# Performance work log

Hardware: AMD Instinct MI355X
Metric: run time of the kernel (lower is better)

## Reference

```python
import jax, jax.numpy as jnp
import numpy as np
import math

B, T, C, H, L, V = 4, 2048, 256, 4, 2, 1024
HS = C // H  # head size


def setup_inputs() -> dict:
    key = jax.random.key(0)
    ks = jax.random.split(key, 10)
    s = 0.02
    return {
        "tokens": jax.random.randint(ks[0], (B, T), 0, V),
        "wte": s * jax.random.normal(ks[1], (V + 1, C), dtype=jnp.float32),
        "ln1_g": jnp.ones((L, C), jnp.float32),
        "ln1_b": jnp.zeros((L, C), jnp.float32),
        "attn_w": s * jax.random.normal(ks[2], (L, 3 * C, C), dtype=jnp.float32),
        "attn_b": jnp.zeros((L, 3 * C), jnp.float32),
        "proj_w": s * jax.random.normal(ks[3], (L, C, C), dtype=jnp.float32),
        "proj_b": jnp.zeros((L, C), jnp.float32),
        "embk": s * jax.random.normal(ks[4], (L, T, HS), dtype=jnp.float32),
        "embv": s * jax.random.normal(ks[5], (L, T, HS), dtype=jnp.float32),
        "ln2_g": jnp.ones((L, C), jnp.float32),
        "ln2_b": jnp.zeros((L, C), jnp.float32),
        "fc_w": s * jax.random.normal(ks[6], (L, 4 * C, C), dtype=jnp.float32),
        "fc_b": jnp.zeros((L, 4 * C), jnp.float32),
        "mproj_w": s * jax.random.normal(ks[7], (L, C, 4 * C), dtype=jnp.float32),
        "mproj_b": jnp.zeros((L, C), jnp.float32),
        "lnf_g": jnp.ones((C,), jnp.float32),
        "lnf_b": jnp.zeros((C,), jnp.float32),
        "head_w": s * jax.random.normal(ks[8], (V, C), dtype=jnp.float32),
    }


def _ln(x, g, b):
    mu = x.mean(-1, keepdims=True)
    var = x.var(-1, keepdims=True)
    return (x - mu) / jnp.sqrt(var + 1e-5) * g + b


def _gelu(x):  # NewGELU (tanh approximation)
    return 0.5 * x * (1.0 + jnp.tanh(math.sqrt(2.0 / math.pi) * (x + 0.044715 * x ** 3)))


def reference(tokens, wte, ln1_g, ln1_b, attn_w, attn_b, proj_w, proj_b,
              embk, embv, ln2_g, ln2_b, fc_w, fc_b, mproj_w, mproj_b,
              lnf_g, lnf_b, head_w):
    x = wte[tokens]  # [B,T,C]; no absolute pos emb in this model
    idx = jnp.arange(T)
    rel = jnp.tril(idx[:, None] - idx[None, :])  # [T,T] nonneg offsets
    causal = idx[:, None] >= idx[None, :]
    scale = 1.0 / math.sqrt(HS)
    for l in range(L):
        h = _ln(x, ln1_g[l], ln1_b[l])
        qkv = h @ attn_w[l].T + attn_b[l]  # [B,T,3C]
        q, k, v = jnp.split(qkv, 3, axis=-1)
        q = q.reshape(B, T, H, HS).transpose(0, 2, 1, 3)  # [B,H,T,hs]
        k = k.reshape(B, T, H, HS).transpose(0, 2, 1, 3)
        v = v.reshape(B, T, H, HS).transpose(0, 2, 1, 3)
        rk = embk[l][rel]  # [T,T,hs]
        rv = embv[l][rel]  # [T,T,hs]
        att = jnp.einsum('bhtd,bhsd->bhts', q, k) * scale \
            + jnp.einsum('bhtd,tsd->bhts', q, rk)
        att = jnp.where(causal, att, -jnp.inf)
        att = jax.nn.softmax(att, axis=-1)
        y = jnp.einsum('bhts,bhsd->bhtd', att, v) \
            + jnp.einsum('bhts,tsd->bhtd', att, rv)
        y = y.transpose(0, 2, 1, 3).reshape(B, T, C)
        x = x + (y @ proj_w[l].T + proj_b[l])
        h2 = _ln(x, ln2_g[l], ln2_b[l])
        x = x + (_gelu(h2 @ fc_w[l].T + fc_b[l]) @ mproj_w[l].T + mproj_b[l])
    x = _ln(x, lnf_g, lnf_b)
    return x @ head_w.T  # [B,T,V] logits
```

## Files before the change

kernel.cpp:

```cpp
#include <hip/hip_runtime.h>
#include <hip/hip_bf16.h>
#include <math.h>

#define BB 4
#define TT 2048
#define CC 256
#define HH 4
#define LL 2
#define VV 1024
#define HS 64
#define EPAD 2176
#define LOG2E 1.4426950408889634f

typedef __attribute__((ext_vector_type(8))) __bf16 bf16x8;
typedef __attribute__((ext_vector_type(4))) float f32x4;

#define MFMA16(a, b, c) __builtin_amdgcn_mfma_f32_16x16x32_bf16((a), (b), (c), 0, 0, 0)

__device__ __forceinline__ ushort f2bf(float f) {
    __hip_bfloat16 h = __float2bfloat16(f);
    return *reinterpret_cast<ushort*>(&h);
}
__device__ __forceinline__ float bf2f(ushort u) {
    union { uint i; float f; } c; c.i = ((uint)u) << 16; return c.f;
}

__device__ __forceinline__ void gload16(const void* g, void* l) {
    __builtin_amdgcn_global_load_lds(
        (const __attribute__((address_space(1))) void*)g,
        (__attribute__((address_space(3))) void*)l, 16, 0, 0);
}

__device__ __forceinline__ float gelu_f(float v) {
    return 0.5f * v * (1.0f + tanhf(0.7978845608028654f * (v + 0.044715f * v * v * v)));
}

__global__ void prep_kernel(const float* __restrict__ w0, const float* __restrict__ w1,
                            const float* __restrict__ w2, const float* __restrict__ w3,
                            const float* __restrict__ w4,
                            ushort* __restrict__ o0, ushort* __restrict__ o1,
                            ushort* __restrict__ o2, ushort* __restrict__ o3,
                            ushort* __restrict__ o4,
                            const float* __restrict__ ek, const float* __restrict__ ev,
                            ushort* __restrict__ ekp, ushort* __restrict__ evtp) {
    int bi = blockIdx.x;
    if (bi < 1792) {
        int i = bi * 256 + threadIdx.x;
        const float* src; ushort* dst; int j;
        if (i < 98304)       { src = w0; dst = o0; j = i; }
        else if (i < 131072) { src = w1; dst = o1; j = i - 98304; }
        else if (i < 262144) { src = w2; dst = o2; j = i - 131072; }
        else if (i < 393216) { src = w3; dst = o3; j = i - 262144; }
        else                 { src = w4; dst = o4; j = i - 393216; }
        float4 v = ((const float4*)src)[j];
        ushort4 o;
        o.x = f2bf(v.x); o.y = f2bf(v.y); o.z = f2bf(v.z); o.w = f2bf(v.w);
        ((ushort4*)dst)[j] = o;
    } else {
        int i = (bi - 1792) * 256 + threadIdx.x;
        int l = i / (EPAD * 64);
        int j = i - l * (EPAD * 64);
        int rp = j >> 6, d = j & 63;
        int o = rp - 64;
        bool in = (o >= 0 && o < TT);
        float kv = in ? ek[(size_t)l * TT * HS + (size_t)o * 64 + d] * LOG2E : 0.0f;
        float vv = in ? ev[(size_t)l * TT * HS + (size_t)o * 64 + d] : 0.0f;
        ekp[(size_t)l * EPAD * 64 + (size_t)rp * 64 + d] = f2bf(kv);
        evtp[(size_t)l * 64 * EPAD + (size_t)d * EPAD + rp] = f2bf(vv);
    }
}

__global__ __launch_bounds__(256) void embed_ln_kernel(
        const int* __restrict__ tok, const float* __restrict__ wte,
        const float* __restrict__ g, const float* __restrict__ b,
        float* __restrict__ x, ushort* __restrict__ h) {
    int row = blockIdx.x * 4 + (threadIdx.x >> 6);
    int lane = threadIdx.x & 63;
    int tk = tok[row];
    float4 v = ((const float4*)(wte + (size_t)tk * CC))[lane];
    float s = v.x + v.y + v.z + v.w;
    float s2 = v.x * v.x + v.y * v.y + v.z * v.z + v.w * v.w;
    for (int m = 1; m < 64; m <<= 1) {
        s += __shfl_xor(s, m);
        s2 += __shfl_xor(s2, m);
    }
    float mean = s * (1.0f / CC);
    float var = s2 * (1.0f / CC) - mean * mean;
    float rs = rsqrtf(var + 1e-5f);
    float4 gg = ((const float4*)g)[lane];
    float4 bb = ((const float4*)b)[lane];
    ushort4 o;
    o.x = f2bf((v.x - mean) * rs * gg.x + bb.x);
    o.y = f2bf((v.y - mean) * rs * gg.y + bb.y);
    o.z = f2bf((v.z - mean) * rs * gg.z + bb.z);
    o.w = f2bf((v.w - mean) * rs * gg.w + bb.w);
    ((float4*)(x + (size_t)row * CC))[lane] = v;
    ((ushort4*)(h + (size_t)row * CC))[lane] = o;
}

template<int MODE>
__global__ __launch_bounds__(512) void bgemm256_kernel(
        const ushort* __restrict__ A, const ushort* __restrict__ W,
        const float* __restrict__ bias, float* __restrict__ out,
        ushort* __restrict__ outb, int N, int K,
        ushort* __restrict__ qb, ushort* __restrict__ kb,
        ushort* __restrict__ vtb) {
    constexpr int BUFSH = 16 * 512;
    __shared__ ushort lds[3 * BUFSH];
    int tid = threadIdx.x;
    int w = tid >> 6, lane = tid & 63;
    int lo = lane & 15, hi = lane >> 4;
    int row0 = blockIdx.y * 128;
    int col0 = blockIdx.x * 128;
    int wm = w >> 2, wn = w & 3;
    const ushort* Asrc = A + (size_t)row0 * K;
    const ushort* Wsrc = W + (size_t)col0 * K;

    auto STAGE = [&](int buf, int k0) {
        ushort* dst = &lds[buf * BUFSH];
        gload16(Asrc + (size_t)(w * 16 + lo) * K + k0 + hi * 8, dst + w * 512);
        gload16(Wsrc + (size_t)(w * 16 + lo) * K + k0 + hi * 8, dst + (8 + w) * 512);
    };

    f32x4 acc[4][2] = {};
    int NT = K >> 5;
    STAGE(0, 0);
    STAGE(1, 32);
    int cur = 0;
    for (int t = 0; t < NT; ++t) {
        if (t + 1 < NT) asm volatile("s_waitcnt vmcnt(2)" ::: "memory");
        else            asm volatile("s_waitcnt vmcnt(0)" ::: "memory");
        __syncthreads();
        if (t + 2 < NT) {
            int st = cur ? cur - 1 : 2;
            STAGE(st, (t + 2) << 5);
        }
        bf16x8 a[4], b[2];
#pragma unroll
        for (int f = 0; f < 4; ++f)
            a[f] = *(const bf16x8*)&lds[cur * BUFSH + (wm * 4 + f) * 512 + lane * 8];
#pragma unroll
        for (int g = 0; g < 2; ++g)
            b[g] = *(const bf16x8*)&lds[cur * BUFSH + (8 + wn * 2 + g) * 512 + lane * 8];
        __builtin_amdgcn_s_setprio(1);
#pragma unroll
        for (int f = 0; f < 4; ++f)
#pragma unroll
            for (int g = 0; g < 2; ++g)
                acc[f][g] = MFMA16(a[f], b[g], acc[f][g]);
        __builtin_amdgcn_s_setprio(0);
        cur = cur < 2 ? cur + 1 : 0;
    }
#pragma unroll
    for (int f = 0; f < 4; ++f) {
        int rr = row0 + wm * 64 + f * 16 + hi * 4;
#pragma unroll
        for (int g = 0; g < 2; ++g) {
            int cc = col0 + wn * 32 + g * 16 + lo;
            float bv = bias ? bias[cc] : 0.0f;
#pragma unroll
            for (int j = 0; j < 4; ++j) {
                int r = rr + j;
                float v = acc[f][g][j] + bv;
                if (MODE == 3) {
                    int t = r & 2047, bb2 = r >> 11;
                    int which = cc >> 8, hh = (cc >> 6) & 3, dd = cc & 63;
                    size_t bh = (size_t)(bb2 * 4 + hh);
                    if (which == 0)      qb[(bh * 2048 + t) * 64 + dd] = f2bf(v);
                    else if (which == 1) kb[(bh * 2048 + t) * 64 + dd] = f2bf(v * (0.125f * LOG2E));
                    else                 vtb[(bh * 64 + dd) * 2048 + t] = f2bf(v);
                } else if (MODE == 2) {
                    outb[(size_t)r * N + cc] = f2bf(gelu_f(v));
                } else {
                    out[(size_t)r * N + cc] = v;
                }
            }
        }
    }
}

template<int NSTEP>
__global__ __launch_bounds__(512) void bgemmln_kernel(
        const ushort* __restrict__ A, const ushort* __restrict__ W,
        const float* __restrict__ bias, float* __restrict__ x,
        const float* __restrict__ lng, const float* __restrict__ lnb,
        ushort* __restrict__ hout) {
    extern __shared__ ushort plds[];
    constexpr int K = NSTEP * 64;
    constexpr int BUFSH = 36 * 512;
    int tid = threadIdx.x;
    int w = tid >> 6, lane = tid & 63;
    int lo = lane & 15, hi = lane >> 4;
    int row0 = blockIdx.x * 32;
    int wm = w >> 2, wn = w & 3;
    const ushort* Asrc = A + (size_t)row0 * K;

    auto STAGE = [&](int buf, int k0) {
        ushort* dst = &plds[buf * BUFSH];
        for (int s = w; s < 36; s += 8) {
            const ushort* src;
            if (s < 4) {
                int rg = s >> 1, kh = s & 1;
                src = Asrc + (size_t)(rg * 16 + lo) * K + k0 + kh * 32 + hi * 8;
            } else {
                int sb = s - 4, cg = sb >> 1, kh = sb & 1;
                src = W + (size_t)(cg * 16 + lo) * K + k0 + kh * 32 + hi * 8;
            }
            gload16(src, dst + s * 512);
        }
    };

    f32x4 acc[4] = {};
    STAGE(0, 0);
    STAGE(1, 64);
    int cur = 0;
    for (int t = 0; t < NSTEP; ++t) {
        if (t + 1 < NSTEP) {
            if (w < 4) asm volatile("s_waitcnt vmcnt(5)" ::: "memory");
            else       asm volatile("s_waitcnt vmcnt(4)" ::: "memory");
        } else {
            asm volatile("s_waitcnt vmcnt(0)" ::: "memory");
        }
        __syncthreads();
        if (t + 2 < NSTEP) {
            int st = cur ? cur - 1 : 2;
            STAGE(st, (t + 2) << 6);
        }
        bf16x8 a[2];
#pragma unroll
        for (int kh = 0; kh < 2; ++kh)
            a[kh] = *(const bf16x8*)&plds[cur * BUFSH + (wm * 2 + kh) * 512 + lane * 8];
        __builtin_amdgcn_s_setprio(1);
#pragma unroll
        for (int g2 = 0; g2 < 4; ++g2) {
#pragma unroll
            for (int kh = 0; kh < 2; ++kh) {
                bf16x8 b = *(const bf16x8*)&plds[cur * BUFSH + 2048 +
                                                 ((wn * 4 + g2) * 2 + kh) * 512 + lane * 8];
                acc[g2] = MFMA16(a[kh], b, acc[g2]);
            }
        }
        __builtin_amdgcn_s_setprio(0);
        cur = cur < 2 ? cur + 1 : 0;
    }

    float* part = (float*)&plds[3 * BUFSH];
    float v[4][4];
    float s1[4] = {0, 0, 0, 0}, s2[4] = {0, 0, 0, 0};
#pragma unroll
    for (int g2 = 0; g2 < 4; ++g2) {
        int cc = wn * 64 + g2 * 16 + lo;
        float bv = bias[cc];
#pragma unroll
        for (int j = 0; j < 4; ++j) {
            int r = row0 + wm * 16 + hi * 4 + j;
            float tv = acc[g2][j] + bv + x[(size_t)r * CC + cc];
            v[g2][j] = tv;
            s1[j] += tv;
            s2[j] += tv * tv;
        }
    }
#pragma unroll
    for (int msk = 1; msk < 16; msk <<= 1)
#pragma unroll
        for (int j = 0; j < 4; ++j) {
            s1[j] += __shfl_xor(s1[j], msk);
            s2[j] += __shfl_xor(s2[j], msk);
        }
    if (lo == 0) {
#pragma unroll
        for (int j = 0; j < 4; ++j) {
            int rr = wm * 16 + hi * 4 + j;
            part[rr * 4 + wn] = s1[j];
            part[128 + rr * 4 + wn] = s2[j];
        }
    }
    __syncthreads();
#pragma unroll
    for (int j = 0; j < 4; ++j) {
        int rr = wm * 16 + hi * 4 + j;
        int r = row0 + rr;
        float4 p1 = *(float4*)&part[rr * 4];
        float4 p2 = *(float4*)&part[128 + rr * 4];
        float mean = (p1.x + p1.y + p1.z + p1.w) * (1.0f / CC);
        float var = (p2.x + p2.y + p2.z + p2.w) * (1.0f / CC) - mean * mean;
        float rsd = rsqrtf(var + 1e-5f);
#pragma unroll
        for (int g2 = 0; g2 < 4; ++g2) {
            int cc = wn * 64 + g2 * 16 + lo;
            x[(size_t)r * CC + cc] = v[g2][j];
            hout[(size_t)r * CC + cc] =
                f2bf((v[g2][j] - mean) * rsd * lng[cc] + lnb[cc]);
        }
    }
}

#define SBUF 57344
#define KOFF 0
#define VOFF 8192
#define EKOFF 16384
#define EVOFF 32768
#define WSCR (2 * SBUF)

__global__ __launch_bounds__(512, 2) void flash_kernel(
        const ushort* __restrict__ qb,
        const ushort* __restrict__ kb,
        const ushort* __restrict__ vtb,
        const ushort* __restrict__ ekp,
        const ushort* __restrict__ evtp,
        ushort* __restrict__ y) {
    extern __shared__ __align__(16) char dls[];

    int g = blockIdx.x;
    int lbid = ((g & 7) << 5) | (g >> 3);
    int bh = lbid >> 4;
    int pk = lbid & 15;
    int tid = threadIdx.x;
    int w = tid >> 6;
    int sub = w & 3;
    int h = w >> 2;
    int lane = tid & 63;
    int lo = lane & 15, hi = lane >> 4;
    int sw = (lo & 7) << 4;

    char* wbase = dls + WSCR + w * 6144;
    ushort (*Rl)[88]   = (ushort (*)[88])  wbase;
    ushort (*Pl)[72]   = (ushort (*)[72])  wbase;
    ushort (*Ppl)[104] = (ushort (*)[104])(wbase + 2816);

    {
        uint* pz = reinterpret_cast<uint*>(&Ppl[0][0]);
        for (int i = lane; i < 832; i += 64) pz[i] = 0;
    }

    const char* kB  = (const char*)(kb  + (size_t)bh * 2048 * 64);
    const char* vB  = (const char*)(vtb + (size_t)bh * 64 * 2048);
    const char* ekB = (const char*)ekp;
    const char* evB = (const char*)evtp;

    int t0A = (31 - pk) * 64, t0B = pk * 64;
    int NSA = 32 - pk;
    const int NC = 33;

    auto STAGE = [&](int buf, int ci) {
        int t0 = (ci < NSA) ? t0A : t0B;
        int s0 = ((ci < NSA) ? ci : ci - NSA) * 64;
        int band0 = t0 - s0;
        char* B = dls + buf * SBUF;
        int wb = (tid & 448) << 4;
        {
            int gb = tid * 16;
            int r = gb >> 7, c = gb & 127;
            gload16(kB + (size_t)(s0 + r) * 128 + (c ^ ((r & 7) << 4)), B + KOFF + wb);
        }
        {
            int gb = tid * 16;
            int r = gb >> 7, c = gb & 127;
            gload16(vB + (size_t)r * 4096 + (size_t)s0 * 2 + (c ^ ((r & 7) << 4)),
                    B + VOFF + wb);
        }
#pragma unroll
        for (int p = 0; p < 2; ++p) {
            int gb = p * 8192 + tid * 16;
            int r = gb >> 7, c = gb & 127;
            gload16(ekB + (size_t)(band0 + r) * 128 + (c ^ ((r & 7) << 4)),
                    B + EKOFF + p * 8192 + wb);
        }
#pragma unroll
        for (int p = 0; p < 3; ++p) {
            int gb = p * 8192 + tid * 16;
            int r = gb / 384, c = gb - r * 384;
            gload16(evB + (size_t)r * 4352 + (size_t)band0 * 2 + (c ^ ((r & 7) << 4)),
                    B + EVOFF + p * 8192 + wb);
        }
    };

    STAGE(0, 0);
    asm volatile("s_waitcnt vmcnt(0)" ::: "memory");
    __syncthreads();

    int b_ = bh >> 2, h_ = bh & 3;
    int buf = 0, ci = 0;
    int nb = h ? 0 : 2;
    int kcA = h ? 0 : 1, kcB = h ? 1 : 2;

    for (int tile = 0; tile < 2; ++tile) {
        int t0 = tile ? t0B : t0A;
        int NS = tile ? (pk + 1) : NSA;

        const ushort* qbase = qb + ((size_t)bh * 2048 + t0 + sub * 16) * 64;
        bf16x8 qf0 = *(const bf16x8*)(qbase + (size_t)lo * 64 + hi * 8);
        bf16x8 qf1 = *(const bf16x8*)(qbase + (size_t)lo * 64 + 32 + hi * 8);

        float rs[4] = {0.0f, 0.0f, 0.0f, 0.0f};
        f32x4 O[4] = {};

        for (int c = 0; c < NS; ++c, ++ci) {
            if (ci + 1 < NC) STAGE(buf ^ 1, ci + 1);
            const char* B = dls + buf * SBUF;
            bool diag = (c == NS - 1);

            f32x4 sacc[2] = {};
            __builtin_amdgcn_s_setprio(1);
#pragma unroll
            for (int ni = 0; ni < 2; ++ni) {
                int R = (2 * h + ni) * 16 + lo;
                bf16x8 b0 = *(const bf16x8*)(B + KOFF + R * 128 + ((hi * 16) ^ sw));
                bf16x8 b1 = *(const bf16x8*)(B + KOFF + R * 128 + ((64 + hi * 16) ^ sw));
                sacc[ni] = MFMA16(qf0, b0, sacc[ni]);
                sacc[ni] = MFMA16(qf1, b1, sacc[ni]);
            }
#pragma unroll
            for (int ni = 0; ni < 3; ++ni) {
                int n = nb + ni;
                int RL = (sub + n) * 16 + lo;
                f32x4 r = {};
                bf16x8 e0 = *(const bf16x8*)(B + EKOFF + RL * 128 + ((hi * 16) ^ sw));
                bf16x8 e1 = *(const bf16x8*)(B + EKOFF + RL * 128 + ((64 + hi * 16) ^ sw));
                r = MFMA16(qf0, e0, r);
                r = MFMA16(qf1, e1, r);
#pragma unroll
                for (int j = 0; j < 4; ++j) Rl[hi * 4 + j][n * 16 + lo] = f2bf(r[j]);
            }
            __builtin_amdgcn_s_setprio(0);
            float sv[2][4];
#pragma unroll
            for (int ni = 0; ni < 2; ++ni) {
                int sl = (2 * h + ni) * 16 + lo;
#pragma unroll
                for (int j = 0; j < 4; ++j) {
                    int r_ = hi * 4 + j;
                    sv[ni][j] = sacc[ni][j] + bf2f(Rl[r_][r_ - sl + 64]);
                }
            }
            asm volatile("" ::: "memory");
#pragma unroll
            for (int ni = 0; ni < 2; ++ni) {
                int sl = (2 * h + ni) * 16 + lo;
#pragma unroll
                for (int j = 0; j < 4; ++j) {
                    int r_ = hi * 4 + j;
                    float p = (!diag || sl <= sub * 16 + r_) ? exp2f(sv[ni][j]) : 0.0f;
                    rs[j] += p;
                    ushort pu = f2bf(p);
                    Pl[r_][sl] = pu;
                    Ppl[r_][r_ - sl + 64] = pu;
                }
            }
            asm volatile("" ::: "memory");

            __builtin_amdgcn_s_setprio(1);
            bf16x8 pa  = *(const bf16x8*)(&Pl[lo][h * 32 + hi * 8]);
            bf16x8 pb0 = *(const bf16x8*)(&Ppl[lo][kcA * 32 + hi * 8]);
            bf16x8 pb1 = *(const bf16x8*)(&Ppl[lo][kcB * 32 + hi * 8]);
#pragma unroll
            for (int n = 0; n < 4; ++n) {
                int R = n * 16 + lo;
                bf16x8 bv = *(const bf16x8*)(B + VOFF + R * 128 + ((h * 64 + hi * 16) ^ sw));
                O[n] = MFMA16(pa, bv, O[n]);
                bf16x8 e0 = *(const bf16x8*)(B + EVOFF + R * 384 +
                                             ((sub * 32 + kcA * 64 + hi * 16) ^ sw));
                O[n] = MFMA16(pb0, e0, O[n]);
                bf16x8 e1 = *(const bf16x8*)(B + EVOFF + R * 384 +
                                             ((sub * 32 + kcB * 64 + hi * 16) ^ sw));
                O[n] = MFMA16(pb1, e1, O[n]);
            }
            __builtin_amdgcn_s_setprio(0);
            asm volatile("" ::: "memory");

            asm volatile("s_waitcnt vmcnt(0)" ::: "memory");
            __syncthreads();
            buf ^= 1;
        }

#pragma unroll
        for (int msk = 1; msk < 16; msk <<= 1)
#pragma unroll
            for (int j = 0; j < 4; ++j) rs[j] += __shfl_xor(rs[j], msk);

        char* mscr = dls + (buf ^ 1) * SBUF + sub * 8192;
        if (h == 1) {
            float* Of = (float*)mscr;
#pragma unroll
            for (int n = 0; n < 4; ++n)
#pragma unroll
                for (int j = 0; j < 4; ++j)
                    Of[(hi * 4 + j) * 64 + n * 16 + lo] = O[n][j];
            if (lo == 0)
#pragma unroll
                for (int j = 0; j < 4; ++j)
                    ((float*)(mscr + 4096))[hi * 4 + j] = rs[j];
        }
        __syncthreads();
        if (h == 0) {
            float* Of = (float*)mscr;
            float inv[4];
#pragma unroll
            for (int j = 0; j < 4; ++j)
                inv[j] = 1.0f / (rs[j] + ((float*)(mscr + 4096))[hi * 4 + j]);
#pragma unroll
            for (int n = 0; n < 4; ++n)
#pragma unroll
                for (int j = 0; j < 4; ++j) {
                    int r = t0 + sub * 16 + hi * 4 + j;
                    float v = O[n][j] + Of[(hi * 4 + j) * 64 + n * 16 + lo];
                    y[((size_t)(b_ * 2048 + r)) * 256 + h_ * 64 + n * 16 + lo] =
                        f2bf(v * inv[j]);
                }
        }
        __syncthreads();
    }
}

extern "C" void kernel_launch(void* const* d_in, const int* in_sizes, int n_in,
                              void* d_out, int out_size, void* d_ws, size_t ws_size,
                              hipStream_t stream) {
    const int*   tokens  = (const int*)d_in[0];
    const float* wte     = (const float*)d_in[1];
    const float* ln1_g   = (const float*)d_in[2];
    const float* ln1_b   = (const float*)d_in[3];
    const float* attn_w  = (const float*)d_in[4];
    const float* attn_b  = (const float*)d_in[5];
    const float* proj_w  = (const float*)d_in[6];
    const float* proj_b  = (const float*)d_in[7];
    const float* embk    = (const float*)d_in[8];
    const float* embv    = (const float*)d_in[9];
    const float* ln2_g   = (const float*)d_in[10];
    const float* ln2_b   = (const float*)d_in[11];
    const float* fc_w    = (const float*)d_in[12];
    const float* fc_b    = (const float*)d_in[13];
    const float* mproj_w = (const float*)d_in[14];
    const float* mproj_b = (const float*)d_in[15];
    const float* lnf_g   = (const float*)d_in[16];
    const float* lnf_b   = (const float*)d_in[17];
    const float* head_w  = (const float*)d_in[18];
    float* out = (float*)d_out;

    const int M = BB * TT;
    char* wsb = (char*)d_ws;
    float*  x    = (float*)wsb;
    ushort* h    = (ushort*)(wsb + ((size_t)8 << 20));
    ushort* y    = (ushort*)(wsb + ((size_t)12 << 20));
    ushort* qb   = (ushort*)(wsb + ((size_t)16 << 20));
    ushort* kbf  = (ushort*)(wsb + ((size_t)20 << 20));
    ushort* vtb  = (ushort*)(wsb + ((size_t)24 << 20));
    ushort* ekp  = (ushort*)(wsb + ((size_t)28 << 20));
    ushort* evtp = ekp + (size_t)LL * EPAD * 64;
    ushort* attn_wb  = (ushort*)(wsb + ((size_t)30 << 20));
    ushort* proj_wb  = attn_wb + (size_t)LL * 3 * CC * CC;
    ushort* fc_wb    = proj_wb + (size_t)LL * CC * CC;
    ushort* mproj_wb = fc_wb + (size_t)LL * 4 * CC * CC;
    ushort* head_wb  = mproj_wb + (size_t)LL * CC * 4 * CC;
    ushort* fcb = (ushort*)d_out;

    dim3 blk(256);
    const int FLDS = WSCR + 8 * 6144;
    const int PLDS = 3 * 36864 + 1024;
    hipFuncSetAttribute(reinterpret_cast<const void*>(flash_kernel),
                        hipFuncAttributeMaxDynamicSharedMemorySize, FLDS);
    hipFuncSetAttribute(reinterpret_cast<const void*>(bgemmln_kernel<4>),
                        hipFuncAttributeMaxDynamicSharedMemorySize, PLDS);
    hipFuncSetAttribute(reinterpret_cast<const void*>(bgemmln_kernel<16>),
                        hipFuncAttributeMaxDynamicSharedMemorySize, PLDS);

    prep_kernel<<<dim3(2880), blk, 0, stream>>>(
        attn_w, proj_w, fc_w, mproj_w, head_w,
        attn_wb, proj_wb, fc_wb, mproj_wb, head_wb,
        embk, embv, ekp, evtp);

    embed_ln_kernel<<<dim3(M / 4), blk, 0, stream>>>(
        tokens, wte, ln1_g, ln1_b, x, h);

    for (int l = 0; l < LL; l++) {
        bgemm256_kernel<3><<<dim3(6, 64), dim3(512), 0, stream>>>(
            h, attn_wb + (size_t)l * 3 * CC * CC, attn_b + (size_t)l * 3 * CC,
            nullptr, nullptr, 3 * CC, CC, qb, kbf, vtb);
        flash_kernel<<<dim3(256), dim3(512), FLDS, stream>>>(
            qb, kbf, vtb, ekp + (size_t)l * EPAD * 64, evtp + (size_t)l * 64 * EPAD, y);
        bgemmln_kernel<4><<<dim3(256), dim3(512), PLDS, stream>>>(
            y, proj_wb + (size_t)l * CC * CC, proj_b + (size_t)l * CC,
            x, ln2_g + l * CC, ln2_b + l * CC, h);
        bgemm256_kernel<2><<<dim3(8, 64), dim3(512), 0, stream>>>(
            h, fc_wb + (size_t)l * 4 * CC * CC, fc_b + (size_t)l * 4 * CC,
            nullptr, fcb, 4 * CC, CC, nullptr, nullptr, nullptr);
        const float* ng = (l == 0) ? (ln1_g + CC) : lnf_g;
        const float* nb = (l == 0) ? (ln1_b + CC) : lnf_b;
        bgemmln_kernel<16><<<dim3(256), dim3(512), PLDS, stream>>>(
            fcb, mproj_wb + (size_t)l * CC * 4 * CC, mproj_b + (size_t)l * CC,
            x, ng, nb, h);
    }

    bgemm256_kernel<0><<<dim3(8, 64), dim3(512), 0, stream>>>(
        h, head_wb, nullptr, out, nullptr, VV, CC, nullptr, nullptr, nullptr);
}
```

Measured before the change: 325.3 us.

## Split KV staging into two phases with finer-grained vmcnt waits

Result: no change. 323.9 us, median of 2 (-0.4%).

```diff
diff --git a/kernel.cpp b/kernel.cpp
--- a/kernel.cpp
+++ b/kernel.cpp
@@ -342,7 +342,7 @@
     int NSA = 32 - pk;
     const int NC = 33;
 
-    auto STAGE = [&](int buf, int ci) {
+    auto STAGE_KE = [&](int buf, int ci) {
         int t0 = (ci < NSA) ? t0A : t0B;
         int s0 = ((ci < NSA) ? ci : ci - NSA) * 64;
         int band0 = t0 - s0;
@@ -353,6 +353,20 @@
             int r = gb >> 7, c = gb & 127;
             gload16(kB + (size_t)(s0 + r) * 128 + (c ^ ((r & 7) << 4)), B + KOFF + wb);
         }
+#pragma unroll
+        for (int p = 0; p < 2; ++p) {
+            int gb = p * 8192 + tid * 16;
+            int r = gb >> 7, c = gb & 127;
+            gload16(ekB + (size_t)(band0 + r) * 128 + (c ^ ((r & 7) << 4)),
+                    B + EKOFF + p * 8192 + wb);
+        }
+    };
+    auto STAGE_VE = [&](int buf, int ci) {
+        int t0 = (ci < NSA) ? t0A : t0B;
+        int s0 = ((ci < NSA) ? ci : ci - NSA) * 64;
+        int band0 = t0 - s0;
+        char* B = dls + buf * SBUF;
+        int wb = (tid & 448) << 4;
         {
             int gb = tid * 16;
             int r = gb >> 7, c = gb & 127;
@@ -360,13 +374,6 @@
                     B + VOFF + wb);
         }
 #pragma unroll
-        for (int p = 0; p < 2; ++p) {
-            int gb = p * 8192 + tid * 16;
-            int r = gb >> 7, c = gb & 127;
-            gload16(ekB + (size_t)(band0 + r) * 128 + (c ^ ((r & 7) << 4)),
-                    B + EKOFF + p * 8192 + wb);
-        }
-#pragma unroll
         for (int p = 0; p < 3; ++p) {
             int gb = p * 8192 + tid * 16;
             int r = gb / 384, c = gb - r * 384;
@@ -375,30 +382,37 @@
         }
     };
 
-    STAGE(0, 0);
-    asm volatile("s_waitcnt vmcnt(0)" ::: "memory");
-    __syncthreads();
+    const ushort* qbaseA = qb + ((size_t)bh * 2048 + t0A + sub * 16) * 64;
+    const ushort* qbaseB = qb + ((size_t)bh * 2048 + t0B + sub * 16) * 64;
+    bf16x8 qfA0 = *(const bf16x8*)(qbaseA + (size_t)lo * 64 + hi * 8);
+    bf16x8 qfA1 = *(const bf16x8*)(qbaseA + (size_t)lo * 64 + 32 + hi * 8);
+    bf16x8 qfB0 = *(const bf16x8*)(qbaseB + (size_t)lo * 64 + hi * 8);
+    bf16x8 qfB1 = *(const bf16x8*)(qbaseB + (size_t)lo * 64 + 32 + hi * 8);
+    STAGE_KE(0, 0);
+    STAGE_VE(0, 0);
 
     int b_ = bh >> 2, h_ = bh & 3;
-    int buf = 0, ci = 0;
+    int ci = 0;
     int nb = h ? 0 : 2;
     int kcA = h ? 0 : 1, kcB = h ? 1 : 2;
 
     for (int tile = 0; tile < 2; ++tile) {
         int t0 = tile ? t0B : t0A;
         int NS = tile ? (pk + 1) : NSA;
-
-        const ushort* qbase = qb + ((size_t)bh * 2048 + t0 + sub * 16) * 64;
-        bf16x8 qf0 = *(const bf16x8*)(qbase + (size_t)lo * 64 + hi * 8);
-        bf16x8 qf1 = *(const bf16x8*)(qbase + (size_t)lo * 64 + 32 + hi * 8);
+        bf16x8 qf0 = tile ? qfB0 : qfA0;
+        bf16x8 qf1 = tile ? qfB1 : qfA1;
 
         float rs[4] = {0.0f, 0.0f, 0.0f, 0.0f};
         f32x4 O[4] = {};
 
         for (int c = 0; c < NS; ++c, ++ci) {
-            if (ci + 1 < NC) STAGE(buf ^ 1, ci + 1);
-            const char* B = dls + buf * SBUF;
+            int cur = ci & 1;
+            const char* B = dls + cur * SBUF;
             bool diag = (c == NS - 1);
+
+            asm volatile("s_waitcnt vmcnt(4)" ::: "memory");
+            __syncthreads();
+            if (ci + 1 < NC) STAGE_KE(cur ^ 1, ci + 1);
 
             f32x4 sacc[2] = {};
             __builtin_amdgcn_s_setprio(1);
@@ -448,6 +462,11 @@
                 }
             }
             asm volatile("" ::: "memory");
+
+            if (ci + 1 < NC) asm volatile("s_waitcnt vmcnt(3)" ::: "memory");
+            else             asm volatile("s_waitcnt vmcnt(0)" ::: "memory");
+            __syncthreads();
+            if (ci + 1 < NC) STAGE_VE(cur ^ 1, ci + 1);
 
             __builtin_amdgcn_s_setprio(1);
             bf16x8 pa  = *(const bf16x8*)(&Pl[lo][h * 32 + hi * 8]);
@@ -467,10 +486,6 @@
             }
             __builtin_amdgcn_s_setprio(0);
             asm volatile("" ::: "memory");
-
-            asm volatile("s_waitcnt vmcnt(0)" ::: "memory");
-            __syncthreads();
-            buf ^= 1;
         }
 
 #pragma unroll
@@ -478,7 +493,8 @@
 #pragma unroll
             for (int j = 0; j < 4; ++j) rs[j] += __shfl_xor(rs[j], msk);
 
-        char* mscr = dls + (buf ^ 1) * SBUF + sub * 8192;
+        char* mscr = dls + ((ci - 1) & 1) * SBUF + sub * 8192;
+        __syncthreads();
         if (h == 1) {
             float* Of = (float*)mscr;
 #pragma unroll
```

## Split flash attention into one query tile per block and read rel-pos embeddings from global

Applied to the files above, without the earlier changes.

Result: slower. 439.0 us (+35.0%).

```diff
diff --git a/kernel.cpp b/kernel.cpp
--- a/kernel.cpp
+++ b/kernel.cpp
@@ -295,14 +295,12 @@
     }
 }
 
-#define SBUF 57344
-#define KOFF 0
-#define VOFF 8192
-#define EKOFF 16384
-#define EVOFF 32768
-#define WSCR (2 * SBUF)
-
-__global__ __launch_bounds__(512, 2) void flash_kernel(
+#define FKOFF 0
+#define FVOFF 8192
+#define FSTG 16384
+#define FWSCR 32768
+
+__global__ __launch_bounds__(512, 4) void flash_kernel(
         const ushort* __restrict__ qb,
         const ushort* __restrict__ kb,
         const ushort* __restrict__ vtb,
@@ -312,9 +310,13 @@
     extern __shared__ __align__(16) char dls[];
 
     int g = blockIdx.x;
-    int lbid = ((g & 7) << 5) | (g >> 3);
-    int bh = lbid >> 4;
-    int pk = lbid & 15;
+    int phase = g >> 8;
+    int pk = (g >> 4) & 15;
+    int bh = g & 15;
+    int tile = phase ? pk : (31 - pk);
+    int t0 = tile * 64;
+    int NS = tile + 1;
+
     int tid = threadIdx.x;
     int w = tid >> 6;
     int sub = w & 3;
@@ -323,7 +325,7 @@
     int lo = lane & 15, hi = lane >> 4;
     int sw = (lo & 7) << 4;
 
-    char* wbase = dls + WSCR + w * 6144;
+    char* wbase = dls + FWSCR + w * 6144;
     ushort (*Rl)[88]   = (ushort (*)[88])  wbase;
     ushort (*Pl)[72]   = (ushort (*)[72])  wbase;
     ushort (*Ppl)[104] = (ushort (*)[104])(wbase + 2816);
@@ -333,182 +335,146 @@
         for (int i = lane; i < 832; i += 64) pz[i] = 0;
     }
 
-    const char* kB  = (const char*)(kb  + (size_t)bh * 2048 * 64);
-    const char* vB  = (const char*)(vtb + (size_t)bh * 64 * 2048);
-    const char* ekB = (const char*)ekp;
-    const char* evB = (const char*)evtp;
-
-    int t0A = (31 - pk) * 64, t0B = pk * 64;
-    int NSA = 32 - pk;
-    const int NC = 33;
-
-    auto STAGE = [&](int buf, int ci) {
-        int t0 = (ci < NSA) ? t0A : t0B;
-        int s0 = ((ci < NSA) ? ci : ci - NSA) * 64;
-        int band0 = t0 - s0;
-        char* B = dls + buf * SBUF;
+    const char* kB = (const char*)(kb + (size_t)bh * 2048 * 64);
+    const char* vB = (const char*)(vtb + (size_t)bh * 64 * 2048);
+
+    auto STAGE_KV = [&](int buf, int s0) {
+        char* B = dls + buf * FSTG;
         int wb = (tid & 448) << 4;
-        {
-            int gb = tid * 16;
-            int r = gb >> 7, c = gb & 127;
-            gload16(kB + (size_t)(s0 + r) * 128 + (c ^ ((r & 7) << 4)), B + KOFF + wb);
-        }
-        {
-            int gb = tid * 16;
-            int r = gb >> 7, c = gb & 127;
-            gload16(vB + (size_t)r * 4096 + (size_t)s0 * 2 + (c ^ ((r & 7) << 4)),
-                    B + VOFF + wb);
-        }
-#pragma unroll
-        for (int p = 0; p < 2; ++p) {
-            int gb = p * 8192 + tid * 16;
-            int r = gb >> 7, c = gb & 127;
-            gload16(ekB + (size_t)(band0 + r) * 128 + (c ^ ((r & 7) << 4)),
-                    B + EKOFF + p * 8192 + wb);
-        }
-#pragma unroll
-        for (int p = 0; p < 3; ++p) {
-            int gb = p * 8192 + tid * 16;
-            int r = gb / 384, c = gb - r * 384;
-            gload16(evB + (size_t)r * 4352 + (size_t)band0 * 2 + (c ^ ((r & 7) << 4)),
-                    B + EVOFF + p * 8192 + wb);
-        }
+        int gb = tid * 16;
+        int r = gb >> 7, c = gb & 127;
+        gload16(kB + (size_t)(s0 + r) * 128 + (c ^ ((r & 7) << 4)), B + FKOFF + wb);
+        gload16(vB + (size_t)r * 4096 + (size_t)s0 * 2 + (c ^ ((r & 7) << 4)),
+                B + FVOFF + wb);
     };
 
-    STAGE(0, 0);
-    asm volatile("s_waitcnt vmcnt(0)" ::: "memory");
-    __syncthreads();
+    const ushort* qbase = qb + ((size_t)bh * 2048 + t0 + sub * 16) * 64;
+    bf16x8 qf0 = *(const bf16x8*)(qbase + (size_t)lo * 64 + hi * 8);
+    bf16x8 qf1 = *(const bf16x8*)(qbase + (size_t)lo * 64 + 32 + hi * 8);
+    STAGE_KV(0, 0);
 
     int b_ = bh >> 2, h_ = bh & 3;
-    int buf = 0, ci = 0;
     int nb = h ? 0 : 2;
     int kcA = h ? 0 : 1, kcB = h ? 1 : 2;
 
-    for (int tile = 0; tile < 2; ++tile) {
-        int t0 = tile ? t0B : t0A;
-        int NS = tile ? (pk + 1) : NSA;
-
-        const ushort* qbase = qb + ((size_t)bh * 2048 + t0 + sub * 16) * 64;
-        bf16x8 qf0 = *(const bf16x8*)(qbase + (size_t)lo * 64 + hi * 8);
-        bf16x8 qf1 = *(const bf16x8*)(qbase + (size_t)lo * 64 + 32 + hi * 8);
-
-        float rs[4] = {0.0f, 0.0f, 0.0f, 0.0f};
-        f32x4 O[4] = {};
-
-        for (int c = 0; c < NS; ++c, ++ci) {
-            if (ci + 1 < NC) STAGE(buf ^ 1, ci + 1);
-            const char* B = dls + buf * SBUF;
-            bool diag = (c == NS - 1);
-
-            f32x4 sacc[2] = {};
-            __builtin_amdgcn_s_setprio(1);
-#pragma unroll
-            for (int ni = 0; ni < 2; ++ni) {
-                int R = (2 * h + ni) * 16 + lo;
-                bf16x8 b0 = *(const bf16x8*)(B + KOFF + R * 128 + ((hi * 16) ^ sw));
-                bf16x8 b1 = *(const bf16x8*)(B + KOFF + R * 128 + ((64 + hi * 16) ^ sw));
-                sacc[ni] = MFMA16(qf0, b0, sacc[ni]);
-                sacc[ni] = MFMA16(qf1, b1, sacc[ni]);
+    float rs[4] = {0.0f, 0.0f, 0.0f, 0.0f};
+    f32x4 O[4] = {};
+
+    for (int c = 0; c < NS; ++c) {
+        int cur = c & 1;
+        const char* B = dls + cur * FSTG;
+        int s0 = c * 64;
+        int band0 = t0 - s0;
+        bool diag = (c == NS - 1);
+
+        asm volatile("s_waitcnt vmcnt(0)" ::: "memory");
+        __syncthreads();
+        if (c + 1 < NS) STAGE_KV(cur ^ 1, s0 + 64);
+
+        f32x4 sacc[2] = {};
+        __builtin_amdgcn_s_setprio(1);
+#pragma unroll
+        for (int ni = 0; ni < 2; ++ni) {
+            int R = (2 * h + ni) * 16 + lo;
+            bf16x8 b0 = *(const bf16x8*)(B + FKOFF + R * 128 + ((hi * 16) ^ sw));
+            bf16x8 b1 = *(const bf16x8*)(B + FKOFF + R * 128 + ((64 + hi * 16) ^ sw));
+            sacc[ni] = MFMA16(qf0, b0, sacc[ni]);
+            sacc[ni] = MFMA16(qf1, b1, sacc[ni]);
+        }
+#pragma unroll
+        for (int ni = 0; ni < 3; ++ni) {
+            int n = nb + ni;
+            int RL = (sub + n) * 16 + lo;
+            const ushort* ekr = ekp + (size_t)(band0 + RL) * 64;
+            bf16x8 e0 = *(const bf16x8*)(ekr + hi * 8);
+            bf16x8 e1 = *(const bf16x8*)(ekr + 32 + hi * 8);
+            f32x4 r = {};
+            r = MFMA16(qf0, e0, r);
+            r = MFMA16(qf1, e1, r);
+#pragma unroll
+            for (int j = 0; j < 4; ++j) Rl[hi * 4 + j][n * 16 + lo] = f2bf(r[j]);
+        }
+        __builtin_amdgcn_s_setprio(0);
+        float sv[2][4];
+#pragma unroll
+        for (int ni = 0; ni < 2; ++ni) {
+            int sl = (2 * h + ni) * 16 + lo;
+#pragma unroll
+            for (int j = 0; j < 4; ++j) {
+                int r_ = hi * 4 + j;
+                sv[ni][j] = sacc[ni][j] + bf2f(Rl[r_][r_ - sl + 64]);
             }
-#pragma unroll
-            for (int ni = 0; ni < 3; ++ni) {
-                int n = nb + ni;
-                int RL = (sub + n) * 16 + lo;
-                f32x4 r = {};
-                bf16x8 e0 = *(const bf16x8*)(B + EKOFF + RL * 128 + ((hi * 16) ^ sw));
-                bf16x8 e1 = *(const bf16x8*)(B + EKOFF + RL * 128 + ((64 + hi * 16) ^ sw));
-                r = MFMA16(qf0, e0, r);
-                r = MFMA16(qf1, e1, r);
-#pragma unroll
-                for (int j = 0; j < 4; ++j) Rl[hi * 4 + j][n * 16 + lo] = f2bf(r[j]);
+        }
+        asm volatile("" ::: "memory");
+#pragma unroll
+        for (int ni = 0; ni < 2; ++ni) {
+            int sl = (2 * h + ni) * 16 + lo;
+#pragma unroll
+            for (int j = 0; j < 4; ++j) {
+                int r_ = hi * 4 + j;
+                float p = (!diag || sl <= sub * 16 + r_) ? exp2f(sv[ni][j]) : 0.0f;
+                rs[j] += p;
+                ushort pu = f2bf(p);
+                Pl[r_][sl] = pu;
+                Ppl[r_][r_ - sl + 64] = pu;
             }
-            __builtin_amdgcn_s_setprio(0);
-            float sv[2][4];
-#pragma unroll
-            for (int ni = 0; ni < 2; ++ni) {
-                int sl = (2 * h + ni) * 16 + lo;
-#pragma unroll
-                for (int j = 0; j < 4; ++j) {
-                    int r_ = hi * 4 + j;
-                    sv[ni][j] = sacc[ni][j] + bf2f(Rl[r_][r_ - sl + 64]);
-                }
+        }
+        asm volatile("" ::: "memory");
+
+        __builtin_amdgcn_s_setprio(1);
+        bf16x8 pa  = *(const bf16x8*)(&Pl[lo][h * 32 + hi * 8]);
+        bf16x8 pb0 = *(const bf16x8*)(&Ppl[lo][kcA * 32 + hi * 8]);
+        bf16x8 pb1 = *(const bf16x8*)(&Ppl[lo][kcB * 32 + hi * 8]);
+#pragma unroll
+        for (int n = 0; n < 4; ++n) {
+            int R = n * 16 + lo;
+            const ushort* evr = evtp + (size_t)R * EPAD + band0 + sub * 16;
+            bf16x8 bv = *(const bf16x8*)(B + FVOFF + R * 128 + ((h * 64 + hi * 16) ^ sw));
+            O[n] = MFMA16(pa, bv, O[n]);
+            bf16x8 e0 = *(const bf16x8*)(evr + kcA * 32 + hi * 8);
+            O[n] = MFMA16(pb0, e0, O[n]);
+            bf16x8 e1 = *(const bf16x8*)(evr + kcB * 32 + hi * 8);
+            O[n] = MFMA16(pb1, e1, O[n]);
+        }
+        __builtin_amdgcn_s_setprio(0);
+        asm volatile("" ::: "memory");
+    }
+
+#pragma unroll
+    for (int msk = 1; msk < 16; msk <<= 1)
+#pragma unroll
+        for (int j = 0; j < 4; ++j) rs[j] += __shfl_xor(rs[j], msk);
+
+    char* mscr = dls + sub * 8192;
+    __syncthreads();
+    if (h == 1) {
+        float* Of = (float*)mscr;
+#pragma unroll
+        for (int n = 0; n < 4; ++n)
+#pragma unroll
+            for (int j = 0; j < 4; ++j)
+                Of[(hi * 4 + j) * 64 + n * 16 + lo] = O[n][j];
+        if (lo == 0)
+#pragma unroll
+            for (int j = 0; j < 4; ++j)
+                ((float*)(mscr + 4096))[hi * 4 + j] = rs[j];
+    }
+    __syncthreads();
+    if (h == 0) {
+        float* Of = (float*)mscr;
+        float inv[4];
+#pragma unroll
+        for (int j = 0; j < 4; ++j)
+            inv[j] = 1.0f / (rs[j] + ((float*)(mscr + 4096))[hi * 4 + j]);
+#pragma unroll
+        for (int n = 0; n < 4; ++n)
+#pragma unroll
+            for (int j = 0; j < 4; ++j) {
+                int r = t0 + sub * 16 + hi * 4 + j;
+                float v = O[n][j] + Of[(hi * 4 + j) * 64 + n * 16 + lo];
+                y[((size_t)(b_ * 2048 + r)) * 256 + h_ * 64 + n * 16 + lo] =
+                    f2bf(v * inv[j]);
             }
-            asm volatile("" ::: "memory");
-#pragma unroll
-            for (int ni = 0; ni < 2; ++ni) {
-                int sl = (2 * h + ni) * 16 + lo;
-#pragma unroll
-                for (int j = 0; j < 4; ++j) {
-                    int r_ = hi * 4 + j;
-                    float p = (!diag || sl <= sub * 16 + r_) ? exp2f(sv[ni][j]) : 0.0f;
-                    rs[j] += p;
-                    ushort pu = f2bf(p);
-                    Pl[r_][sl] = pu;
-                    Ppl[r_][r_ - sl + 64] = pu;
-                }
-            }
-            asm volatile("" ::: "memory");
-
-            __builtin_amdgcn_s_setprio(1);
-            bf16x8 pa  = *(const bf16x8*)(&Pl[lo][h * 32 + hi * 8]);
-            bf16x8 pb0 = *(const bf16x8*)(&Ppl[lo][kcA * 32 + hi * 8]);
-            bf16x8 pb1 = *(const bf16x8*)(&Ppl[lo][kcB * 32 + hi * 8]);
-#pragma unroll
-            for (int n = 0; n < 4; ++n) {
-                int R = n * 16 + lo;
-                bf16x8 bv = *(const bf16x8*)(B + VOFF + R * 128 + ((h * 64 + hi * 16) ^ sw));
-                O[n] = MFMA16(pa, bv, O[n]);
-                bf16x8 e0 = *(const bf16x8*)(B + EVOFF + R * 384 +
-                                             ((sub * 32 + kcA * 64 + hi * 16) ^ sw));
-                O[n] = MFMA16(pb0, e0, O[n]);
-                bf16x8 e1 = *(const bf16x8*)(B + EVOFF + R * 384 +
-                                             ((sub * 32 + kcB * 64 + hi * 16) ^ sw));
-                O[n] = MFMA16(pb1, e1, O[n]);
-            }
-            __builtin_amdgcn_s_setprio(0);
-            asm volatile("" ::: "memory");
-
-            asm volatile("s_waitcnt vmcnt(0)" ::: "memory");
-            __syncthreads();
-            buf ^= 1;
-        }
-
-#pragma unroll
-        for (int msk = 1; msk < 16; msk <<= 1)
-#pragma unroll
-            for (int j = 0; j < 4; ++j) rs[j] += __shfl_xor(rs[j], msk);
-
-        char* mscr = dls + (buf ^ 1) * SBUF + sub * 8192;
-        if (h == 1) {
-            float* Of = (float*)mscr;
-#pragma unroll
-            for (int n = 0; n < 4; ++n)
-#pragma unroll
-                for (int j = 0; j < 4; ++j)
-                    Of[(hi * 4 + j) * 64 + n * 16 + lo] = O[n][j];
-            if (lo == 0)
-#pragma unroll
-                for (int j = 0; j < 4; ++j)
-                    ((float*)(mscr + 4096))[hi * 4 + j] = rs[j];
-        }
-        __syncthreads();
-        if (h == 0) {
-            float* Of = (float*)mscr;
-            float inv[4];
-#pragma unroll
-            for (int j = 0; j < 4; ++j)
-                inv[j] = 1.0f / (rs[j] + ((float*)(mscr + 4096))[hi * 4 + j]);
-#pragma unroll
-            for (int n = 0; n < 4; ++n)
-#pragma unroll
-                for (int j = 0; j < 4; ++j) {
-                    int r = t0 + sub * 16 + hi * 4 + j;
-                    float v = O[n][j] + Of[(hi * 4 + j) * 64 + n * 16 + lo];
-                    y[((size_t)(b_ * 2048 + r)) * 256 + h_ * 64 + n * 16 + lo] =
-                        f2bf(v * inv[j]);
-                }
-        }
-        __syncthreads();
     }
 }
 
@@ -554,7 +520,7 @@
     ushort* fcb = (ushort*)d_out;
 
     dim3 blk(256);
-    const int FLDS = WSCR + 8 * 6144;
+    const int FLDS = FWSCR + 8 * 6144;
     const int PLDS = 3 * 36864 + 1024;
     hipFuncSetAttribute(reinterpret_cast<const void*>(flash_kernel),
                         hipFuncAttributeMaxDynamicSharedMemorySize, FLDS);
@@ -575,7 +541,7 @@
         bgemm256_kernel<3><<<dim3(6, 64), dim3(512), 0, stream>>>(
             h, attn_wb + (size_t)l * 3 * CC * CC, attn_b + (size_t)l * 3 * CC,
             nullptr, nullptr, 3 * CC, CC, qb, kbf, vtb);
-        flash_kernel<<<dim3(256), dim3(512), FLDS, stream>>>(
+        flash_kernel<<<dim3(512), dim3(512), FLDS, stream>>>(
             qb, kbf, vtb, ekp + (size_t)l * EPAD * 64, evtp + (size_t)l * 64 * EPAD, y);
         bgemmln_kernel<4><<<dim3(256), dim3(512), PLDS, stream>>>(
             y, proj_wb + (size_t)l * CC * CC, proj_b + (size_t)l * CC,
```
